# Optimization experiments

Hardware: AMD Instinct MI355X
Metric: run time of the kernel (lower is better)

The kernel has to match this reference:

```python
import jax, jax.numpy as jnp
import numpy as np

B, U1, U2 = 2, 3072, 3072
IF = 256      # in_feat_dim
FD = 256      # feat_dim
M = 4         # num_modes
D = IF // M   # attention_mode_dim = 64
STD = 0.02    # base_initializer_range
LN_EPS = 1e-12


def setup_inputs() -> dict:
    key = jax.random.key(0)
    ks = jax.random.split(key, 8)
    inp = {
        'query_feat': jax.random.normal(ks[0], (B, U1, IF), jnp.float32),
        'key_feat':   jax.random.normal(ks[1], (B, U2, IF), jnp.float32),
        # tied QK projection (key weight == query weight after tie_qk)
        'Wq':    jax.random.normal(ks[2], (M * D, IF), jnp.float32) * STD,
        # value projection of ExpandedFeatTrans.first_linear (v_has_bias=True)
        'Wv':    jax.random.normal(ks[3], (M * FD, IF), jnp.float32) * STD,
        'bv':    jnp.zeros((M * FD,), jnp.float32),
        # MMSharedMid shared linear
        'W_mid': jax.random.normal(ks[4], (FD, FD), jnp.float32) * STD,
        'b_mid': jnp.zeros((FD,), jnp.float32),
        # MMSharedOutput shared linear + LayerNorm
        'W_out': jax.random.normal(ks[5], (FD, FD), jnp.float32) * STD,
        'b_out': jnp.zeros((FD,), jnp.float32),
        'ln_g':  jnp.ones((FD,), jnp.float32),
        'ln_b':  jnp.zeros((FD,), jnp.float32),
        # LearnedSoftAggregate feat2score linear (FD -> 1)
        'W_agg': jax.random.normal(ks[6], (1, FD), jnp.float32) * STD,
        'b_agg': jnp.zeros((1,), jnp.float32),
    }
    return inp


def _layer_norm(x, g, b):
    mu = x.mean(-1, keepdims=True)
    var = ((x - mu) ** 2).mean(-1, keepdims=True)
    return (x - mu) * jax.lax.rsqrt(var + LN_EPS) * g + b


def reference(query_feat, key_feat, Wq, Wv, bv, W_mid, b_mid, W_out, b_out,
              ln_g, ln_b, W_agg, b_agg):
    # --- multi-mode cross attention with tied QK ---
    q = (query_feat @ Wq.T).reshape(B, U1, M, D).transpose(0, 2, 1, 3)  # b m u d
    k = (key_feat   @ Wq.T).reshape(B, U2, M, D).transpose(0, 2, 1, 3)  # b m v d
    scores = jnp.einsum('bmud,bmvd->bmuv', q, k) / np.float32(np.sqrt(D))
    probs = jax.nn.softmax(scores, axis=-1)                              # b m u v

    # --- ExpandedFeatTrans: per-mode value projection + fusion ---
    v = (key_feat @ Wv.T + bv).reshape(B, U2, M, FD).transpose(0, 2, 1, 3)  # b m v f
    fused = jnp.einsum('bmuv,bmvf->bmuf', probs, v)                          # b m u f

    # --- MMSharedMid FFN (shared linear + exact gelu; dropout=0) ---
    mid = jax.nn.gelu(fused @ W_mid.T + b_mid, approximate=False)

    # --- MMSharedOutput: shared linear + residual + LayerNorm ---
    outp = _layer_norm(mid @ W_out.T + b_out + fused, ln_g, ln_b)            # b m u f

    # --- LearnedSoftAggregate over modes (group_dim=1) ---
    mode_scores = (outp @ W_agg.T + b_agg)[..., 0]                           # b m u
    agg_probs = jax.nn.softmax(mode_scores, axis=1)
    trans_feat = (outp * agg_probs[..., None]).sum(axis=1)                   # b u f
    return trans_feat
```

## Files before the change

### kernel.cpp

```cpp
#include <hip/hip_runtime.h>
#include <hip/hip_bf16.h>
#include <cstdint>
#include <cstddef>

typedef __attribute__((ext_vector_type(8))) short     bf16x8;
typedef __attribute__((ext_vector_type(4))) float     f32x4;
typedef __attribute__((ext_vector_type(4))) unsigned short u16x4;

using as1_void = __attribute__((address_space(1))) void;
using as3_void = __attribute__((address_space(3))) void;

#define MFMA16(a,b,c) __builtin_amdgcn_mfma_f32_16x16x32_bf16((a),(b),(c),0,0,0)

__device__ __forceinline__ unsigned short f2bf(float f) {
  union { float f; unsigned u; } v; v.f = f;
  unsigned r = v.u + 0x7fffu + ((v.u >> 16) & 1u);
  return (unsigned short)(r >> 16);
}
__device__ __forceinline__ float bf2f(unsigned short h) {
  union { unsigned u; float f; } v; v.u = ((unsigned)h) << 16; return v.f;
}
__device__ __forceinline__ unsigned cvt_pk_bf16(float lo, float hi) {
  unsigned r;
  asm volatile("v_cvt_pk_bf16_f32 %0, %1, %2" : "=v"(r) : "v"(lo), "v"(hi));
  return r;
}

__device__ __forceinline__ void gload16(const void* g, void* l) {
  __builtin_amdgcn_global_load_lds((const as1_void*)g, (as3_void*)l, 16, 0, 0);
}

constexpr size_t oXq  = 0;
constexpr size_t oXk  = oXq + 1572864ull * 2;
constexpr size_t oWq  = oXk + 1572864ull * 2;
constexpr size_t oWv  = oWq + 65536ull   * 2;
constexpr size_t oWm  = oWv + 262144ull  * 2;
constexpr size_t oWo  = oWm + 65536ull   * 2;
constexpr size_t oQb  = oWo + 65536ull   * 2;
constexpr size_t oKb  = oQb + 1572864ull * 2;
constexpr size_t oVb  = oKb + 1572864ull * 2;
constexpr size_t oPa  = oVb + 6291456ull * 2;
constexpr size_t oMl  = oPa + 12582912ull * 2;

__global__ __launch_bounds__(256) void cvtw_kernel(
    const float* __restrict__ wq, const float* __restrict__ wv,
    const float* __restrict__ wm, const float* __restrict__ wo,
    char* __restrict__ wsb) {
  int i4 = (blockIdx.x * 256 + threadIdx.x) * 4;
  const float* src; size_t dsto; int local;
  if (i4 < 65536)        { src = wq; dsto = oWq; local = i4; }
  else if (i4 < 327680)  { src = wv; dsto = oWv; local = i4 - 65536; }
  else if (i4 < 393216)  { src = wm; dsto = oWm; local = i4 - 327680; }
  else                   { src = wo; dsto = oWo; local = i4 - 393216; }
  f32x4 v = *(const f32x4*)(src + local);
  u16x4 o;
  o.x = f2bf(v.x); o.y = f2bf(v.y); o.z = f2bf(v.z); o.w = f2bf(v.w);
  *(u16x4*)((unsigned short*)(wsb + dsto) + local) = o;
}

__global__ __launch_bounds__(256, 2) void proj_kernel(
    const float* __restrict__ qf32, const float* __restrict__ kf32,
    const float* __restrict__ bv, char* __restrict__ wsb) {
  __shared__ unsigned short sA[64 * 256];

  const int lane = threadIdx.x & 63, wid = threadIdx.x >> 6;
  const int lq = lane & 15, hi = lane >> 4;
  const int ny = blockIdx.x % 6;
  const int r0 = (blockIdx.x / 6) * 64;

  const float* Xf = (ny == 0) ? qf32 : kf32;
  const unsigned short* W;
  if (ny <= 1) W = (const unsigned short*)(wsb + oWq);
  else         W = (const unsigned short*)(wsb + oWv) + (size_t)(ny - 2) * 256 * 256;

  {
    const int t = threadIdx.x;
#pragma unroll
    for (int j = 0; j < 16; ++j) {
      int flat = j * 256 + t;
      int row = flat >> 6;
      int c4 = flat & 63;
      f32x4 v = *(const f32x4*)(Xf + ((size_t)(r0 + row) * 256 + c4 * 4));
      u16x4 o;
      o.x = f2bf(v.x); o.y = f2bf(v.y); o.z = f2bf(v.z); o.w = f2bf(v.w);
      int col = c4 * 4;
      int c8 = col >> 3;
      *(u16x4*)&sA[row * 256 + (((c8 ^ (row & 7)) << 3) + (col & 7))] = o;
    }
  }
  __syncthreads();

  const int n0 = wid * 64;

  f32x4 acc[4][4];
#pragma unroll
  for (int rg = 0; rg < 4; ++rg)
#pragma unroll
    for (int bt = 0; bt < 4; ++bt) acc[rg][bt] = (f32x4){0.f, 0.f, 0.f, 0.f};

#pragma unroll
  for (int ks = 0; ks < 8; ++ks) {
    bf16x8 a[4];
#pragma unroll
    for (int rg = 0; rg < 4; ++rg)
      a[rg] = *(const bf16x8*)&sA[(rg * 16 + lq) * 256 + (((ks * 4 + hi) ^ (lq & 7)) << 3)];
#pragma unroll
    for (int bt = 0; bt < 4; ++bt) {
      int n = n0 + bt * 16 + lq;
      bf16x8 bfr = *(const bf16x8*)(W + (size_t)n * 256 + ks * 32 + hi * 8);
#pragma unroll
      for (int rg = 0; rg < 4; ++rg) acc[rg][bt] = MFMA16(a[rg], bfr, acc[rg][bt]);
    }
  }

  const int b = r0 / 3072, u0 = r0 % 3072;

  if (ny <= 1) {
    unsigned short* outp = (unsigned short*)(wsb + (ny == 0 ? oQb : oKb));
    float scale = (ny == 0) ? 0.125f : 1.0f;
    int m = wid;
#pragma unroll
    for (int bt = 0; bt < 4; ++bt) {
      int d = bt * 16 + lq;
#pragma unroll
      for (int rg = 0; rg < 4; ++rg) {
        int ub = u0 + rg * 16 + hi * 4;
#pragma unroll
        for (int r = 0; r < 4; ++r) {
          outp[((size_t)(b * 4 + m) * 3072 + (ub + r)) * 64 + d] = f2bf(acc[rg][bt][r] * scale);
        }
      }
    }
  } else {
    unsigned short* vbT = (unsigned short*)(wsb + oVb);
    int mchunk = ny - 2;
#pragma unroll
    for (int bt = 0; bt < 4; ++bt) {
      int f = n0 + bt * 16 + lq;
      float bias = bv[mchunk * 256 + f];
#pragma unroll
      for (int rg = 0; rg < 4; ++rg) {
        int ub = u0 + rg * 16 + hi * 4;
        u16x4 pk;
#pragma unroll
        for (int r = 0; r < 4; ++r) pk[r] = f2bf(acc[rg][bt][r] + bias);
        *(u16x4*)(vbT + ((size_t)(b * 4 + mchunk) * 256 + f) * 3072 + ub) = pk;
      }
    }
  }
}

__global__ __launch_bounds__(256, 3) void attn_kernel(char* __restrict__ wsb) {
  __shared__ unsigned short sK[64 * 64];
  __shared__ unsigned short sV[256 * 64];
  __shared__ unsigned short sP[4][16 * 64];
  __shared__ float sCr[4];
  __shared__ float sInv[4][16];

  const int lane = threadIdx.x & 63, wid = threadIdx.x >> 6;
  const int lq = lane & 15, hi = lane >> 4;
  const int lr3 = lane >> 3, lc3 = lane & 7;
  const int fh = wid >> 1, gp = wid & 1;
  const int bm = blockIdx.x & 7;
  const int z = blockIdx.x >> 3;
  const int qt = z >> 1, kvh = z & 1;
  const int q0 = qt * 64;
  const int kvbase = kvh * 1536;
  const int key = lq & 7;

  const unsigned short* qb = (const unsigned short*)(wsb + oQb) + (size_t)bm * 3072 * 64;
  const unsigned short* kb = (const unsigned short*)(wsb + oKb) + (size_t)bm * 3072 * 64;
  const unsigned short* vb = (const unsigned short*)(wsb + oVb) + (size_t)bm * 256 * 3072;

  const unsigned short* qp = qb + (size_t)(q0 + wid * 16 + lq) * 64 + hi * 8;
  const bf16x8 qf0 = *(const bf16x8*)(qp);
  const bf16x8 qf1 = *(const bf16x8*)(qp + 32);
  asm volatile("s_waitcnt vmcnt(0)" ::: "memory");

  const unsigned short* pk[2];
  unsigned short* dk[2];
#pragma unroll
  for (int i = 0; i < 2; ++i) {
    int ch = wid * 2 + i;
    int r = ch * 8 + lr3;
    int cs = lc3 ^ (r & 7);
    pk[i] = kb + (size_t)(kvbase + r) * 64 + cs * 8;
    dk[i] = &sK[ch * 512];
  }
  const unsigned short* pv[8];
  unsigned short* dv[8];
#pragma unroll
  for (int i = 0; i < 8; ++i) {
    int ch = i * 4 + wid;
    int f = ch * 8 + lr3;
    int cs = lc3 ^ (f & 7);
    pv[i] = vb + (size_t)f * 3072 + kvbase + cs * 8;
    dv[i] = &sV[ch * 512];
  }

  f32x4 acc[2][8];
#pragma unroll
  for (int g = 0; g < 2; ++g)
#pragma unroll
    for (int ft = 0; ft < 8; ++ft) acc[g][ft] = (f32x4){0.f, 0.f, 0.f, 0.f};
  float mrun = -1e30f, lrun = 0.f;

  char* myP = (char*)&sP[wid][0];
  const int g0 = gp * 2, g1 = gp * 2 + 1;
  char* rP0 = (char*)&sP[g0][0];
  char* rP1 = (char*)&sP[g1][0];

  gload16(pk[0], dk[0]); gload16(pk[1], dk[1]);
  pk[0] += 4096; pk[1] += 4096;

  for (int kt = 0; kt < 24; ++kt) {
#pragma unroll
    for (int i = 0; i < 8; ++i) { gload16(pv[i], dv[i]); pv[i] += 64; }

    asm volatile("s_waitcnt vmcnt(8)" ::: "memory");
    __builtin_amdgcn_sched_barrier(0);
    __builtin_amdgcn_s_barrier();

    bf16x8 kc0[4], kc1[4];
#pragma unroll
    for (int t = 0; t < 4; ++t) {
      const unsigned short* kr = &sK[(t * 16 + lq) * 64];
      kc0[t] = *(const bf16x8*)(kr + ((hi ^ key) * 8));
      kc1[t] = *(const bf16x8*)(kr + (((hi + 4) ^ key) * 8));
    }
    f32x4 s[4];
#pragma unroll
    for (int t = 0; t < 4; ++t) {
      f32x4 zz = (f32x4){0.f, 0.f, 0.f, 0.f};
      zz = MFMA16(kc0[t], qf0, zz);
      zz = MFMA16(kc1[t], qf1, zz);
      s[t] = zz;
    }

    float pmax = s[0][0];
#pragma unroll
    for (int t = 0; t < 4; ++t)
#pragma unroll
      for (int r = 0; r < 4; ++r) pmax = fmaxf(pmax, s[t][r]);
    pmax = fmaxf(pmax, __shfl_xor(pmax, 16));
    pmax = fmaxf(pmax, __shfl_xor(pmax, 32));

    float cr = 1.0f;
    if (__any(pmax > mrun + 8.0f)) {
      float mnew = fmaxf(mrun, pmax);
      cr = __builtin_amdgcn_exp2f((mrun - mnew) * 1.44269504f);
      lrun *= cr; mrun = mnew;
    }
    if (lane == 0) sCr[wid] = cr;

    const float mk = mrun * 1.44269504f;
    float ps[4][4];
    float psum = 0.f;
#pragma unroll
    for (int t = 0; t < 4; ++t)
#pragma unroll
      for (int r = 0; r < 4; ++r) {
        float p = __builtin_amdgcn_exp2f(s[t][r] * 1.44269504f - mk);
        ps[t][r] = p; psum += p;
      }
    psum += __shfl_xor(psum, 16);
    psum += __shfl_xor(psum, 32);
    lrun += psum;

#pragma unroll
    for (int t = 0; t < 4; ++t) {
      unsigned w0 = cvt_pk_bf16(ps[t][0], ps[t][1]);
      unsigned w1 = cvt_pk_bf16(ps[t][2], ps[t][3]);
      int c = (2 * t + (hi >> 1)) ^ key;
      *(uint2*)(myP + lq * 128 + (c << 4) + ((hi & 1) << 3)) = make_uint2(w0, w1);
    }

    asm volatile("s_waitcnt vmcnt(0) lgkmcnt(0)" ::: "memory");
    __builtin_amdgcn_sched_barrier(0);
    __builtin_amdgcn_s_barrier();

    if (kt < 23) {
      gload16(pk[0], dk[0]); gload16(pk[1], dk[1]);
      pk[0] += 4096; pk[1] += 4096;
    }

    float c0 = sCr[g0], c1 = sCr[g1];
    if (c0 != 1.0f) {
#pragma unroll
      for (int ft = 0; ft < 8; ++ft) {
        acc[0][ft][0] *= c0; acc[0][ft][1] *= c0;
        acc[0][ft][2] *= c0; acc[0][ft][3] *= c0;
      }
    }
    if (c1 != 1.0f) {
#pragma unroll
      for (int ft = 0; ft < 8; ++ft) {
        acc[1][ft][0] *= c1; acc[1][ft][1] *= c1;
        acc[1][ft][2] *= c1; acc[1][ft][3] *= c1;
      }
    }

    bf16x8 pb00 = *(const bf16x8*)(rP0 + lq * 128 + ((hi ^ key) << 4));
    bf16x8 pb01 = *(const bf16x8*)(rP0 + lq * 128 + (((4 + hi) ^ key) << 4));
    bf16x8 pb10 = *(const bf16x8*)(rP1 + lq * 128 + ((hi ^ key) << 4));
    bf16x8 pb11 = *(const bf16x8*)(rP1 + lq * 128 + (((4 + hi) ^ key) << 4));

    __builtin_amdgcn_s_setprio(1);
#pragma unroll
    for (int ft = 0; ft < 8; ++ft) {
      const unsigned short* vr = &sV[(fh * 128 + ft * 16 + lq) * 64];
      bf16x8 vf0 = *(const bf16x8*)(vr + ((hi ^ key) * 8));
      bf16x8 vf1 = *(const bf16x8*)(vr + (((4 + hi) ^ key) * 8));
      acc[0][ft] = MFMA16(vf0, pb00, acc[0][ft]);
      acc[0][ft] = MFMA16(vf1, pb01, acc[0][ft]);
      acc[1][ft] = MFMA16(vf0, pb10, acc[1][ft]);
      acc[1][ft] = MFMA16(vf1, pb11, acc[1][ft]);
    }
    __builtin_amdgcn_s_setprio(0);

    asm volatile("s_waitcnt lgkmcnt(0)" ::: "memory");
    __builtin_amdgcn_sched_barrier(0);
    __builtin_amdgcn_s_barrier();
  }

  if (hi == 0) {
    sInv[wid][lq] = 1.0f / lrun;
    float* ml = (float*)(wsb + oMl);
    size_t qi = (size_t)(kvh * 8 + bm) * 3072 + q0 + wid * 16 + lq;
    *(float2*)(ml + qi * 2) = make_float2(mrun, lrun);
  }
  __syncthreads();

  unsigned short* paB = (unsigned short*)(wsb + oPa) + (size_t)(kvh * 8 + bm) * 3072 * 256;
#pragma unroll
  for (int gi = 0; gi < 2; ++gi) {
    int g = gp * 2 + gi;
    float inv = sInv[g][lq];
    unsigned short* orow = paB + (size_t)(q0 + g * 16 + lq) * 256 + fh * 128 + hi * 4;
#pragma unroll
    for (int ft = 0; ft < 8; ++ft) {
      u16x4 pk4;
#pragma unroll
      for (int r = 0; r < 4; ++r) pk4[r] = f2bf(acc[gi][ft][r] * inv);
      *(u16x4*)(orow + ft * 16) = pk4;
    }
  }
}

__global__ __launch_bounds__(256, 3) void ffn_kernel(char* __restrict__ wsb,
                                                     const float* __restrict__ bmid,
                                                     const float* __restrict__ bout,
                                                     const float* __restrict__ lng,
                                                     const float* __restrict__ lnb,
                                                     const float* __restrict__ wagg,
                                                     const float* __restrict__ bagg,
                                                     float* __restrict__ out) {
  __shared__ unsigned short sA[32 * 256];
  __shared__ unsigned short sM[32 * 256];
  __shared__ float redS[4][32], redQ[4][32], redC[4][32];
  __shared__ float sSc[32];
  __shared__ float sW0[32], sW1[32];

  const int lane = threadIdx.x & 63, wid = threadIdx.x >> 6;
  const int lq = lane & 15, hi = lane >> 4;
  const int b = blockIdx.x / 384;
  const int u0 = (blockIdx.x % 384) * 8;

  const unsigned short* Wm = (const unsigned short*)(wsb + oWm);
  const unsigned short* Wo = (const unsigned short*)(wsb + oWo);
  const unsigned short* pa = (const unsigned short*)(wsb + oPa);
  const float* mlb = (const float*)(wsb + oMl);

  if (threadIdx.x < 32) {
    int m = threadIdx.x & 3, du = threadIdx.x >> 2;
    size_t qi = (size_t)(b * 4 + m) * 3072 + u0 + du;
    float2 ml0 = *(const float2*)(mlb + qi * 2);
    float2 ml1 = *(const float2*)(mlb + (qi + 8ull * 3072) * 2);
    float M = fmaxf(ml0.x, ml1.x);
    float e0 = ml0.y * __builtin_amdgcn_exp2f((ml0.x - M) * 1.44269504f);
    float e1 = ml1.y * __builtin_amdgcn_exp2f((ml1.x - M) * 1.44269504f);
    float inv = 1.0f / (e0 + e1);
    sW0[threadIdx.x] = e0 * inv;
    sW1[threadIdx.x] = e1 * inv;
  }
  __syncthreads();

  {
    int t = threadIdx.x;
#pragma unroll
    for (int j = 0; j < 4; ++j) {
      int i = j * 256 + t;
      int row = i >> 5, c = i & 31;
      int m = row & 3, du = row >> 2;
      const unsigned short* p0 = pa + ((size_t)(b * 4 + m) * 3072 + u0 + du) * 256 + c * 8;
      bf16x8 a = *(const bf16x8*)(p0);
      bf16x8 bb = *(const bf16x8*)(p0 + 8ull * 3072 * 256);
      float w0 = sW0[row], w1 = sW1[row];
      u16x4 oA, oB;
#pragma unroll
      for (int e = 0; e < 4; ++e) {
        oA[e] = f2bf(w0 * bf2f((unsigned short)a[e]) + w1 * bf2f((unsigned short)bb[e]));
        oB[e] = f2bf(w0 * bf2f((unsigned short)a[e + 4]) + w1 * bf2f((unsigned short)bb[e + 4]));
      }
      unsigned short* dst = &sA[row * 256 + ((c ^ (row & 7)) << 3)];
      *(u16x4*)(dst) = oA;
      *(u16x4*)(dst + 4) = oB;
    }
  }
  __syncthreads();

  const int n0 = wid * 64;
  const int rowb = hi * 4;

  f32x4 acc1[2][4];
#pragma unroll
  for (int rg = 0; rg < 2; ++rg)
#pragma unroll
    for (int bt = 0; bt < 4; ++bt) acc1[rg][bt] = (f32x4){0.f, 0.f, 0.f, 0.f};
#pragma unroll
  for (int ks = 0; ks < 8; ++ks) {
    bf16x8 a[2];
#pragma unroll
    for (int rg = 0; rg < 2; ++rg)
      a[rg] = *(const bf16x8*)&sA[(rg * 16 + lq) * 256 + (((ks * 4 + hi) ^ (lq & 7)) << 3)];
#pragma unroll
    for (int bt = 0; bt < 4; ++bt) {
      int n = n0 + bt * 16 + lq;
      bf16x8 bfr = *(const bf16x8*)(Wm + (size_t)n * 256 + ks * 32 + hi * 8);
#pragma unroll
      for (int rg = 0; rg < 2; ++rg) acc1[rg][bt] = MFMA16(a[rg], bfr, acc1[rg][bt]);
    }
  }
#pragma unroll
  for (int bt = 0; bt < 4; ++bt) {
    int n = n0 + bt * 16 + lq;
    float bb = bmid[n];
#pragma unroll
    for (int rg = 0; rg < 2; ++rg)
#pragma unroll
      for (int r = 0; r < 4; ++r) {
        float x = acc1[rg][bt][r] + bb;
        float g = 0.5f * x * (1.0f + erff(x * 0.7071067811865475f));
        int row = rg * 16 + rowb + r;
        sM[row * 256 + (((n >> 3) ^ (row & 7)) << 3) + (n & 7)] = f2bf(g);
      }
  }
  __syncthreads();

  f32x4 acc2[2][4];
#pragma unroll
  for (int rg = 0; rg < 2; ++rg)
#pragma unroll
    for (int bt = 0; bt < 4; ++bt) acc2[rg][bt] = (f32x4){0.f, 0.f, 0.f, 0.f};
#pragma unroll
  for (int ks = 0; ks < 8; ++ks) {
    bf16x8 a[2];
#pragma unroll
    for (int rg = 0; rg < 2; ++rg)
      a[rg] = *(const bf16x8*)&sM[(rg * 16 + lq) * 256 + (((ks * 4 + hi) ^ (lq & 7)) << 3)];
#pragma unroll
    for (int bt = 0; bt < 4; ++bt) {
      int n = n0 + bt * 16 + lq;
      bf16x8 bfr = *(const bf16x8*)(Wo + (size_t)n * 256 + ks * 32 + hi * 8);
#pragma unroll
      for (int rg = 0; rg < 2; ++rg) acc2[rg][bt] = MFMA16(a[rg], bfr, acc2[rg][bt]);
    }
  }

  float sS[2][4], sQ[2][4];
#pragma unroll
  for (int rg = 0; rg < 2; ++rg)
#pragma unroll
    for (int r = 0; r < 4; ++r) { sS[rg][r] = 0.f; sQ[rg][r] = 0.f; }
#pragma unroll
  for (int bt = 0; bt < 4; ++bt) {
    int n = n0 + bt * 16 + lq;
    float bo = bout[n];
#pragma unroll
    for (int rg = 0; rg < 2; ++rg)
#pragma unroll
      for (int r = 0; r < 4; ++r) {
        int row = rg * 16 + rowb + r;
        float res = bf2f(sA[row * 256 + (((n >> 3) ^ (row & 7)) << 3) + (n & 7)]);
        float x = acc2[rg][bt][r] + bo + res;
        acc2[rg][bt][r] = x;
        sS[rg][r] += x;
        sQ[rg][r] += x * x;
      }
  }
#pragma unroll
  for (int rg = 0; rg < 2; ++rg)
#pragma unroll
    for (int r = 0; r < 4; ++r) {
#pragma unroll
      for (int off = 1; off < 16; off <<= 1) {
        sS[rg][r] += __shfl_xor(sS[rg][r], off);
        sQ[rg][r] += __shfl_xor(sQ[rg][r], off);
      }
    }
  if (lq == 0) {
#pragma unroll
    for (int rg = 0; rg < 2; ++rg)
#pragma unroll
      for (int r = 0; r < 4; ++r) {
        int row = rg * 16 + rowb + r;
        redS[wid][row] = sS[rg][r]; redQ[wid][row] = sQ[rg][r];
      }
  }
  __syncthreads();

  float scp[2][4];
#pragma unroll
  for (int rg = 0; rg < 2; ++rg)
#pragma unroll
    for (int r = 0; r < 4; ++r) {
      int row = rg * 16 + rowb + r;
      float ts = redS[0][row] + redS[1][row] + redS[2][row] + redS[3][row];
      float tq = redQ[0][row] + redQ[1][row] + redQ[2][row] + redQ[3][row];
      float mean = ts * (1.0f / 256.0f);
      float var = tq * (1.0f / 256.0f) - mean * mean;
      float rs = rsqrtf(var + 1e-12f);
      float sc = 0.f;
#pragma unroll
      for (int bt = 0; bt < 4; ++bt) {
        int n = n0 + bt * 16 + lq;
        float o = (acc2[rg][bt][r] - mean) * rs * lng[n] + lnb[n];
        acc2[rg][bt][r] = o;
        sc += o * wagg[n];
      }
      scp[rg][r] = sc;
    }
#pragma unroll
  for (int rg = 0; rg < 2; ++rg)
#pragma unroll
    for (int r = 0; r < 4; ++r) {
#pragma unroll
      for (int off = 1; off < 16; off <<= 1) scp[rg][r] += __shfl_xor(scp[rg][r], off);
    }
  if (lq == 0) {
#pragma unroll
    for (int rg = 0; rg < 2; ++rg)
#pragma unroll
      for (int r = 0; r < 4; ++r) redC[wid][rg * 16 + rowb + r] = scp[rg][r];
  }
  __syncthreads();

  if (threadIdx.x < 32) {
    int t = threadIdx.x;
    sSc[t] = redC[0][t] + redC[1][t] + redC[2][t] + redC[3][t] + bagg[0];
  }
  __syncthreads();

  float wm[2][4];
#pragma unroll
  for (int rg = 0; rg < 2; ++rg) {
    int du = rg * 4 + hi;
    float s0 = sSc[du * 4 + 0], s1 = sSc[du * 4 + 1];
    float s2 = sSc[du * 4 + 2], s3 = sSc[du * 4 + 3];
    float mx = fmaxf(fmaxf(s0, s1), fmaxf(s2, s3));
    float e0 = __builtin_amdgcn_exp2f((s0 - mx) * 1.44269504f);
    float e1 = __builtin_amdgcn_exp2f((s1 - mx) * 1.44269504f);
    float e2 = __builtin_amdgcn_exp2f((s2 - mx) * 1.44269504f);
    float e3 = __builtin_amdgcn_exp2f((s3 - mx) * 1.44269504f);
    float inv = 1.0f / (e0 + e1 + e2 + e3);
    wm[rg][0] = e0 * inv; wm[rg][1] = e1 * inv;
    wm[rg][2] = e2 * inv; wm[rg][3] = e3 * inv;
  }
#pragma unroll
  for (int bt = 0; bt < 4; ++bt) {
    int n = n0 + bt * 16 + lq;
#pragma unroll
    for (int rg = 0; rg < 2; ++rg) {
      int du = rg * 4 + hi;
      float val = wm[rg][0] * acc2[rg][bt][0] + wm[rg][1] * acc2[rg][bt][1]
                + wm[rg][2] * acc2[rg][bt][2] + wm[rg][3] * acc2[rg][bt][3];
      out[((size_t)(b * 3072 + u0 + du)) * 256 + n] = val;
    }
  }
}

extern "C" void kernel_launch(void* const* d_in, const int* in_sizes, int n_in,
                              void* d_out, int out_size, void* d_ws, size_t ws_size,
                              hipStream_t stream) {
  const float* q  = (const float*)d_in[0];
  const float* k  = (const float*)d_in[1];
  const float* wq = (const float*)d_in[2];
  const float* wv = (const float*)d_in[3];
  const float* bv = (const float*)d_in[4];
  const float* wm = (const float*)d_in[5];
  const float* bm = (const float*)d_in[6];
  const float* wo = (const float*)d_in[7];
  const float* bo = (const float*)d_in[8];
  const float* lg = (const float*)d_in[9];
  const float* lb = (const float*)d_in[10];
  const float* wa = (const float*)d_in[11];
  const float* ba = (const float*)d_in[12];
  char* wsb = (char*)d_ws;

  cvtw_kernel<<<448, 256, 0, stream>>>(wq, wv, wm, wo, wsb);
  proj_kernel<<<576, 256, 0, stream>>>(q, k, bv, wsb);
  attn_kernel<<<768, 256, 0, stream>>>(wsb);
  ffn_kernel<<<768, 256, 0, stream>>>(wsb, bm, bo, lg, lb, wa, ba, (float*)d_out);
}
```

Before: 129.4 us.

## Load K tiles directly into registers and use polynomial erf in GELU

The attention kernel no longer stages K tiles through shared memory. Each wave loads its K fragments straight from global memory into registers and prefetches the next tile after the mid-loop barrier, which removes one barrier, one vmcnt wait and the LDS reads per iteration. Separately, the exact erff in the GELU epilogue is replaced with an Abramowitz-Stegun polynomial that uses hardware rcp/exp2. That cuts transcendental cost but gives only about 1e-7 absolute accuracy, and the direct K loads add register pressure and expose global latency.

Result: slower. 178.0 us (+37.5%).

```diff
diff --git a/kernel.cpp b/kernel.cpp
--- a/kernel.cpp
+++ b/kernel.cpp
@@ -24,6 +24,18 @@
   unsigned r;
   asm volatile("v_cvt_pk_bf16_f32 %0, %1, %2" : "=v"(r) : "v"(lo), "v"(hi));
   return r;
+}
+__device__ __forceinline__ float fast_erf(float x) {
+  float ax = fabsf(x);
+  float t = __builtin_amdgcn_rcpf(fmaf(0.3275911f, ax, 1.0f));
+  float p = fmaf(1.061405429f, t, -1.453152027f);
+  p = fmaf(p, t, 1.421413741f);
+  p = fmaf(p, t, -0.284496736f);
+  p = fmaf(p, t, 0.254829592f);
+  p = p * t;
+  float e = __builtin_amdgcn_exp2f(-ax * ax * 1.44269504f);
+  float r = fmaf(-p, e, 1.0f);
+  return copysignf(r, x);
 }
 
 __device__ __forceinline__ void gload16(const void* g, void* l) {
@@ -151,7 +163,6 @@
 }
 
 __global__ __launch_bounds__(256, 3) void attn_kernel(char* __restrict__ wsb) {
-  __shared__ unsigned short sK[64 * 64];
   __shared__ unsigned short sV[256 * 64];
   __shared__ unsigned short sP[4][16 * 64];
   __shared__ float sCr[4];
@@ -177,16 +188,6 @@
   const bf16x8 qf1 = *(const bf16x8*)(qp + 32);
   asm volatile("s_waitcnt vmcnt(0)" ::: "memory");
 
-  const unsigned short* pk[2];
-  unsigned short* dk[2];
-#pragma unroll
-  for (int i = 0; i < 2; ++i) {
-    int ch = wid * 2 + i;
-    int r = ch * 8 + lr3;
-    int cs = lc3 ^ (r & 7);
-    pk[i] = kb + (size_t)(kvbase + r) * 64 + cs * 8;
-    dk[i] = &sK[ch * 512];
-  }
   const unsigned short* pv[8];
   unsigned short* dv[8];
 #pragma unroll
@@ -198,6 +199,8 @@
     dv[i] = &sV[ch * 512];
   }
 
+  const unsigned short* kp = kb + (size_t)(kvbase + lq) * 64 + hi * 8;
+
   f32x4 acc[2][8];
 #pragma unroll
   for (int g = 0; g < 2; ++g)
@@ -210,24 +213,18 @@
   char* rP0 = (char*)&sP[g0][0];
   char* rP1 = (char*)&sP[g1][0];
 
-  gload16(pk[0], dk[0]); gload16(pk[1], dk[1]);
-  pk[0] += 4096; pk[1] += 4096;
+  bf16x8 kc0[4], kc1[4];
+#pragma unroll
+  for (int t = 0; t < 4; ++t) {
+    kc0[t] = *(const bf16x8*)(kp + (size_t)t * 1024);
+    kc1[t] = *(const bf16x8*)(kp + (size_t)t * 1024 + 32);
+  }
+  kp += 4096;
 
   for (int kt = 0; kt < 24; ++kt) {
 #pragma unroll
     for (int i = 0; i < 8; ++i) { gload16(pv[i], dv[i]); pv[i] += 64; }
 
-    asm volatile("s_waitcnt vmcnt(8)" ::: "memory");
-    __builtin_amdgcn_sched_barrier(0);
-    __builtin_amdgcn_s_barrier();
-
-    bf16x8 kc0[4], kc1[4];
-#pragma unroll
-    for (int t = 0; t < 4; ++t) {
-      const unsigned short* kr = &sK[(t * 16 + lq) * 64];
-      kc0[t] = *(const bf16x8*)(kr + ((hi ^ key) * 8));
-      kc1[t] = *(const bf16x8*)(kr + (((hi + 4) ^ key) * 8));
-    }
     f32x4 s[4];
 #pragma unroll
     for (int t = 0; t < 4; ++t) {
@@ -280,8 +277,12 @@
     __builtin_amdgcn_s_barrier();
 
     if (kt < 23) {
-      gload16(pk[0], dk[0]); gload16(pk[1], dk[1]);
-      pk[0] += 4096; pk[1] += 4096;
+#pragma unroll
+      for (int t = 0; t < 4; ++t) {
+        kc0[t] = *(const bf16x8*)(kp + (size_t)t * 1024);
+        kc1[t] = *(const bf16x8*)(kp + (size_t)t * 1024 + 32);
+      }
+      kp += 4096;
     }
 
     float c0 = sCr[g0], c1 = sCr[g1];
@@ -440,7 +441,7 @@
 #pragma unroll
       for (int r = 0; r < 4; ++r) {
         float x = acc1[rg][bt][r] + bb;
-        float g = 0.5f * x * (1.0f + erff(x * 0.7071067811865475f));
+        float g = 0.5f * x * (1.0f + fast_erf(x * 0.7071067811865475f));
         int row = rg * 16 + rowb + r;
         sM[row * 256 + (((n >> 3) ^ (row & 7)) << 3) + (n & 7)] = f2bf(g);
       }
```
